# Kernel tuning notes

Measured on AMD Instinct MI355X. Metric: run time of the kernel, lower is better.

The kernel has to match this reference:

```python
import jax, jax.numpy as jnp
import numpy as np

B, N, F, H, HEADS = 2, 256, 64, 64, 4
C = HEADS * H  # n_coefficients (coefficients_mlp is Identity => must equal n_heads*hidden)
EPS = 1e-5
INF = 1e5


def _lin(key, fan_in, fan_out, bias=True):
    k1, k2 = jax.random.split(key)
    w = jax.random.normal(k1, (fan_in, fan_out), jnp.float32) * (1.0 / np.sqrt(fan_in))
    if bias:
        b = jax.random.normal(k2, (fan_out,), jnp.float32) * 0.01
        return w, b
    return w


def setup_inputs() -> dict:
    key = jax.random.key(0)
    ks = jax.random.split(key, 16)
    inp = dict(
        h=jax.random.normal(ks[0], (B, N, F), jnp.float32),
        x=jax.random.normal(ks[1], (B, N, 3), jnp.float32),
        v=jax.random.normal(ks[2], (B, N, 3), jnp.float32),
    )
    inp['edge_w1'], inp['edge_b1'] = _lin(ks[3], 2 * F + 1, H)
    inp['edge_w2'], inp['edge_b2'] = _lin(ks[4], H, H)
    inp['sem_w'], inp['sem_b'] = _lin(ks[5], H, HEADS)
    inp['post_w1'], inp['post_b1'] = _lin(ks[6], C, H)
    inp['post_w2'], inp['post_b2'] = _lin(ks[7], H, H)
    inp['node_w1'], inp['node_b1'] = _lin(ks[8], C + H + F, H)
    inp['node_w2'], inp['node_b2'] = _lin(ks[9], H, F)
    inp['vel_w1'], inp['vel_b1'] = _lin(ks[10], F, H)
    inp['vel_w2'] = _lin(ks[11], H, 1, bias=False) * 0.001  # xavier gain=0.001 analogue
    inp['vmix_w'] = _lin(ks[12], C, 1, bias=False)[:, 0]
    inp['log_gamma'] = -jnp.log(jnp.linspace(1.0, 5.0, HEADS)).astype(jnp.float32)
    return inp


def reference(h, x, v, edge_w1, edge_b1, edge_w2, edge_b2, sem_w, sem_b,
              post_w1, post_b1, post_w2, post_b2, node_w1, node_b1,
              node_w2, node_b2, vel_w1, vel_b1, vel_w2, vmix_w, log_gamma):
    silu = jax.nn.silu
    n = h.shape[-2]
    eye = jnp.eye(n, dtype=h.dtype)[:, :, None]  # [N,N,1] diagonal mask

    # pairwise geometry: entry [i,j] = x_j - x_i
    x_minus_xt = x[..., None, :, :] - x[..., :, None, :]                # [B,N,N,3]
    x_norm = jnp.sqrt((x_minus_xt ** 2).sum(-1, keepdims=True) + EPS)   # [B,N,N,1]

    # pairwise node-feature concat (h_j, h_i) + distance -> edge MLP
    h_j = jnp.broadcast_to(h[..., None, :, :], (B, n, n, F))
    h_i = jnp.broadcast_to(h[..., :, None, :], (B, n, n, F))
    h_cat = jnp.concatenate([h_j, h_i, x_norm], axis=-1)                # [B,N,N,2F+1]
    h_e_mtx = silu(silu(h_cat @ edge_w1 + edge_b1) @ edge_w2 + edge_b2)  # [B,N,N,H]

    # euclidean attention: softmin over j of gamma*dist, diagonal masked out
    dist = (x_norm + INF * eye) * jnp.exp(log_gamma)                    # [B,N,N,heads]
    euclid_att = jax.nn.softmax(-dist, axis=-2)
    # semantic attention: LeakyReLU(0.2) logits, diagonal masked, softmax over j
    sem = jax.nn.leaky_relu(h_e_mtx @ sem_w + sem_b, 0.2) - INF * eye
    sem_att = jax.nn.softmax(sem, axis=-2)
    comb_att = jax.nn.softmax(euclid_att * sem_att, axis=-2)            # [B,N,N,heads]

    # attention-weighted edge features, flattened over (H, heads)
    h_e_att = (h_e_mtx[..., :, None] * comb_att[..., None, :]).reshape(B, n, n, C)

    # spatial attention (coefficients_mlp is Identity)
    unit = x_minus_xt / (x_norm + EPS)                                  # [B,N,N,3]
    # combinations.mean(dim=-3) without materializing [B,N,N,C,3]
    comb_sum = jnp.einsum('bijc,bijd->bicd', h_e_att, unit) / n         # [B,N,C,3]
    comb_norm = (comb_sum ** 2).sum(-1)                                 # [B,N,C]
    h_comb = silu(silu(comb_norm @ post_w1 + post_b1) @ post_w2 + post_b2)

    # delta_v = mean_j (v_mixing over C of combinations)
    delta_v = jnp.einsum('bijc,c,bijd->bid', h_e_att, vmix_w, unit) / n  # [B,N,3]

    h_agg = h_e_att.sum(axis=-2)                                        # sum over j -> [B,N,C]
    out = jnp.concatenate([h, h_agg, h_comb], axis=-1)
    out = silu(silu(out @ node_w1 + node_b1) @ node_w2 + node_b2)
    h_new = h + out                                                     # residual

    # coordinate / velocity update
    v_scale = silu(h_new @ vel_w1 + vel_b1) @ vel_w2                    # [B,N,1]
    v_new = delta_v + v_scale * v
    x_new = x + v_new
    return h_new, x_new, v_new
```

## Files before the change

kernel.cpp:

```cpp
#include <hip/hip_runtime.h>
#include <hip/hip_bf16.h>
#include <math.h>

#define EPSV 1e-5f
#define INFV 1e5f

typedef short bf16x8 __attribute__((ext_vector_type(8)));
typedef float f32x4 __attribute__((ext_vector_type(4)));

__device__ __forceinline__ float rcp_f(float x) { return __builtin_amdgcn_rcpf(x); }
__device__ __forceinline__ float silu_f(float v) { return v * rcp_f(1.0f + __expf(-v)); }

__device__ __forceinline__ unsigned short f2bf(float f) {
  unsigned int u = __float_as_uint(f);
  u = (u + 0x7fffu + ((u >> 16) & 1u)) >> 16;
  return (unsigned short)u;
}
__device__ __forceinline__ float bf2f(unsigned short h) {
  return __uint_as_float(((unsigned int)h) << 16);
}
__device__ __forceinline__ unsigned int pkbf(float a, float b) {
  float2 f2; f2.x = a; f2.y = b;
  __hip_bfloat162 t = __float22bfloat162_rn(f2);
  unsigned int u;
  __builtin_memcpy(&u, &t, 4);
  return u;
}

__device__ __forceinline__ float4 br4(float4 v, int op, float4* sc) {
  const int tid = threadIdx.x;
#pragma unroll
  for (int off = 32; off >= 1; off >>= 1) {
    float ox = __shfl_xor(v.x, off);
    float oy = __shfl_xor(v.y, off);
    float oz = __shfl_xor(v.z, off);
    float ow = __shfl_xor(v.w, off);
    if (op) { v.x = fmaxf(v.x, ox); v.y = fmaxf(v.y, oy); v.z = fmaxf(v.z, oz); v.w = fmaxf(v.w, ow); }
    else    { v.x += ox; v.y += oy; v.z += oz; v.w += ow; }
  }
  if ((tid & 63) == 0) sc[tid >> 6] = v;
  __syncthreads();
  float4 r0 = sc[0], r1 = sc[1], r2 = sc[2], r3 = sc[3];
  if (op) {
    v.x = fmaxf(fmaxf(r0.x, r1.x), fmaxf(r2.x, r3.x));
    v.y = fmaxf(fmaxf(r0.y, r1.y), fmaxf(r2.y, r3.y));
    v.z = fmaxf(fmaxf(r0.z, r1.z), fmaxf(r2.z, r3.z));
    v.w = fmaxf(fmaxf(r0.w, r1.w), fmaxf(r2.w, r3.w));
  } else {
    v.x = r0.x + r1.x + r2.x + r3.x;
    v.y = r0.y + r1.y + r2.y + r3.y;
    v.z = r0.z + r1.z + r2.z + r3.z;
    v.w = r0.w + r1.w + r2.w + r3.w;
  }
  __syncthreads();
  return v;
}

__device__ __forceinline__ void gemm64(const unsigned short* TH, const unsigned short* E2T,
                                       int w, int l15, int quad, f32x4 acc[4][4]) {
#pragma unroll
  for (int tr = 0; tr < 4; ++tr)
#pragma unroll
    for (int tc = 0; tc < 4; ++tc)
      acc[tr][tc] = (f32x4){0.f, 0.f, 0.f, 0.f};
#pragma unroll
  for (int ms = 0; ms < 64; ms += 32) {
    bf16x8 af[4], bfr[4];
#pragma unroll
    for (int tr = 0; tr < 4; ++tr)
      af[tr] = *reinterpret_cast<const bf16x8*>(&TH[(64 * w + 16 * tr + l15) * 72 + ms + quad * 8]);
#pragma unroll
    for (int tc = 0; tc < 4; ++tc)
      bfr[tc] = *reinterpret_cast<const bf16x8*>(&E2T[(16 * tc + l15) * 72 + ms + quad * 8]);
#pragma unroll
    for (int tr = 0; tr < 4; ++tr)
#pragma unroll
      for (int tc = 0; tc < 4; ++tc)
        acc[tr][tc] = __builtin_amdgcn_mfma_f32_16x16x32_bf16(af[tr], bfr[tc], acc[tr][tc], 0, 0, 0);
  }
}

__global__ __launch_bounds__(256, 3) void k_all(
    const float* __restrict__ h, const float* __restrict__ x, const float* __restrict__ v,
    const float* __restrict__ ew1, const float* __restrict__ eb1,
    const float* __restrict__ ew2, const float* __restrict__ eb2,
    const float* __restrict__ semw, const float* __restrict__ semb,
    const float* __restrict__ pw1, const float* __restrict__ pb1,
    const float* __restrict__ pw2, const float* __restrict__ pb2,
    const float* __restrict__ nw1, const float* __restrict__ nb1,
    const float* __restrict__ nw2, const float* __restrict__ nb2,
    const float* __restrict__ vw1, const float* __restrict__ vb1,
    const float* __restrict__ vw2, const float* __restrict__ vmix,
    const float* __restrict__ lgam, float* __restrict__ out) {

  __shared__ __align__(16) unsigned short TH[256 * 72];
  __shared__ __align__(16) char E2u[9216];
  __shared__ __align__(16) float4 unit_l[256];
  __shared__ float addk[64];
  __shared__ float w1dk[64];
  __shared__ __align__(16) float bms[256];

  unsigned short* E2T = (unsigned short*)E2u;
  float*  sd    = (float*)E2u;
  float4* cat_l = (float4*)E2u;
  float*  cn_l  = (float*)(E2u + 4096);
  float*  hag_l = (float*)(E2u + 5120);
  float4* sc    = (float4*)(E2u + 8192);
  float*  dvs   = (float*)(E2u + 8320);
  float* tmp = (float*)TH;
  float* m1s = (float*)TH + 256;
  float* hnw = (float*)TH + 320;
  float* nin = (float*)TH + 384;

  const int bi  = blockIdx.x;
  const int i   = bi & 255;
  const int b0  = bi & ~255;
  const int tid = threadIdx.x;
  const int j   = tid;
  const int bj  = b0 | j;

  const float xi0 = x[bi * 3 + 0], xi1 = x[bi * 3 + 1], xi2 = x[bi * 3 + 2];
  const float dx = x[bj * 3 + 0] - xi0;
  const float dy = x[bj * 3 + 1] - xi1;
  const float dz = x[bj * 3 + 2] - xi2;
  const float dn = sqrtf(dx * dx + dy * dy + dz * dz + EPSV);
  const float invn = rcp_f(dn + EPSV);
  const float ux = dx * invn, uy = dy * invn, uz = dz * invn;
  unit_l[j] = make_float4(ux, uy, uz, dn);

  {
    const float4* hb4 = reinterpret_cast<const float4*>(h + (size_t)b0 * 64);
#pragma unroll
    for (int q = 0; q < 16; ++q) {
      int idx = q * 256 + tid;
      float4 f4 = hb4[idx];
      int row = idx >> 4, c4 = idx & 15;
      uint2 pk;
      pk.x = pkbf(f4.x, f4.y);
      pk.y = pkbf(f4.z, f4.w);
      *reinterpret_cast<uint2*>(&TH[row * 72 + c4 * 4]) = pk;
    }
  }
#pragma unroll
  for (int q = 0; q < 16; ++q) {
    int idx = q * 256 + tid;
    E2T[(idx & 63) * 72 + (idx >> 6)] = f2bf(ew1[idx]);
  }
  {
    int s = tid >> 6, k = tid & 63;
    const float* hrow = h + (size_t)bi * 64;
    float bp = 0.f;
#pragma unroll
    for (int f2 = 0; f2 < 16; ++f2) {
      int f = s * 16 + f2;
      bp += hrow[f] * ew1[(64 + f) * 64 + k];
    }
    bms[s * 64 + k] = bp;
  }
  __syncthreads();
  if (tid < 64) {
    addk[tid] = eb1[tid] + bms[tid] + bms[64 + tid] + bms[128 + tid] + bms[192 + tid];
    w1dk[tid] = ew1[128 * 64 + tid];
  }

  const int lid  = tid & 63;
  const int w    = tid >> 6;
  const int l15  = lid & 15;
  const int quad = lid >> 4;

  f32x4 acc[4][4];
  gemm64(TH, E2T, w, l15, quad, acc);
  __syncthreads();

#pragma unroll
  for (int tc = 0; tc < 4; ++tc) {
    float ak = addk[16 * tc + l15];
    float wd = w1dk[16 * tc + l15];
#pragma unroll
    for (int tr = 0; tr < 4; ++tr)
#pragma unroll
      for (int r = 0; r < 4; ++r) {
        int row = 64 * w + 16 * tr + quad * 4 + r;
        float val = silu_f(acc[tr][tc][r] + ak + unit_l[row].w * wd);
        TH[row * 72 + 16 * tc + l15] = f2bf(val);
      }
  }
#pragma unroll
  for (int q = 0; q < 16; ++q) {
    int idx = q * 256 + tid;
    E2T[(idx & 63) * 72 + (idx >> 6)] = f2bf(ew2[idx]);
  }
  __syncthreads();

  gemm64(TH, E2T, w, l15, quad, acc);
  __syncthreads();

#pragma unroll
  for (int tc = 0; tc < 4; ++tc) {
    float b2 = eb2[16 * tc + l15];
#pragma unroll
    for (int tr = 0; tr < 4; ++tr)
#pragma unroll
      for (int r = 0; r < 4; ++r) {
        int row = 64 * w + 16 * tr + quad * 4 + r;
        TH[row * 72 + 16 * tc + l15] = f2bf(silu_f(acc[tr][tc][r] + b2));
      }
  }
#pragma unroll
  for (int q = 0; q < 2; ++q) {
    int idx = q * 256 + tid;
    int n = idx >> 6, kk = idx & 63;
    float wv = (n < 4) ? semw[kk * 4 + n] : vmix[kk * 4 + (n - 4)];
    E2T[n * 72 + kk] = f2bf(wv);
  }
  __syncthreads();

  f32x4 acc3[4];
  {
#pragma unroll
    for (int tr = 0; tr < 4; ++tr) acc3[tr] = (f32x4){0.f, 0.f, 0.f, 0.f};
#pragma unroll
    for (int ms = 0; ms < 64; ms += 32) {
      bf16x8 b3 = *reinterpret_cast<const bf16x8*>(&E2T[l15 * 72 + ms + quad * 8]);
#pragma unroll
      for (int tr = 0; tr < 4; ++tr) {
        bf16x8 a3 = *reinterpret_cast<const bf16x8*>(&TH[(64 * w + 16 * tr + l15) * 72 + ms + quad * 8]);
        acc3[tr] = __builtin_amdgcn_mfma_f32_16x16x32_bf16(a3, b3, acc3[tr], 0, 0, 0);
      }
    }
  }
  __syncthreads();
  if (l15 < 8) {
#pragma unroll
    for (int tr = 0; tr < 4; ++tr)
#pragma unroll
      for (int r = 0; r < 4; ++r)
        sd[(64 * w + 16 * tr + quad * 4 + r) * 8 + l15] = acc3[tr][r];
  }
  __syncthreads();

  float4 s01 = *reinterpret_cast<const float4*>(sd + j * 8);
  float4 s23 = *reinterpret_cast<const float4*>(sd + j * 8 + 4);
  float4 sbv = *reinterpret_cast<const float4*>(semb);
  const float diag = (j == i) ? INFV : 0.0f;
  float4 sl;
  sl.x = s01.x + sbv.x; sl.y = s01.y + sbv.y; sl.z = s01.z + sbv.z; sl.w = s01.w + sbv.w;
  sl.x = ((sl.x > 0.f) ? sl.x : 0.2f * sl.x) - diag;
  sl.y = ((sl.y > 0.f) ? sl.y : 0.2f * sl.y) - diag;
  sl.z = ((sl.z > 0.f) ? sl.z : 0.2f * sl.z) - diag;
  sl.w = ((sl.w > 0.f) ? sl.w : 0.2f * sl.w) - diag;

  float4 lg = *reinterpret_cast<const float4*>(lgam);
  const float dni = dn + diag;
  float4 e_eu = make_float4(__expf(-dni * __expf(lg.x)), __expf(-dni * __expf(lg.y)),
                            __expf(-dni * __expf(lg.z)), __expf(-dni * __expf(lg.w)));

  float4 M = br4(sl, 1, sc);
  float4 e_sem = make_float4(__expf(sl.x - M.x), __expf(sl.y - M.y),
                             __expf(sl.z - M.z), __expf(sl.w - M.w));

  float4 a8 = e_eu, b8 = e_sem;
#pragma unroll
  for (int off = 32; off >= 1; off >>= 1) {
    a8.x += __shfl_xor(a8.x, off); a8.y += __shfl_xor(a8.y, off);
    a8.z += __shfl_xor(a8.z, off); a8.w += __shfl_xor(a8.w, off);
    b8.x += __shfl_xor(b8.x, off); b8.y += __shfl_xor(b8.y, off);
    b8.z += __shfl_xor(b8.z, off); b8.w += __shfl_xor(b8.w, off);
  }
  if ((tid & 63) == 0) { sc[tid >> 6] = a8; sc[4 + (tid >> 6)] = b8; }
  __syncthreads();
  float4 Se, Ss;
  {
    float4 r0 = sc[0], r1 = sc[1], r2 = sc[2], r3 = sc[3];
    Se = make_float4(r0.x + r1.x + r2.x + r3.x, r0.y + r1.y + r2.y + r3.y,
                     r0.z + r1.z + r2.z + r3.z, r0.w + r1.w + r2.w + r3.w);
    float4 s0 = sc[4], s1 = sc[5], s2 = sc[6], s3 = sc[7];
    Ss = make_float4(s0.x + s1.x + s2.x + s3.x, s0.y + s1.y + s2.y + s3.y,
                     s0.z + s1.z + s2.z + s3.z, s0.w + s1.w + s2.w + s3.w);
  }
  __syncthreads();

  float4 p = make_float4((e_eu.x * rcp_f(Se.x)) * (e_sem.x * rcp_f(Ss.x)),
                         (e_eu.y * rcp_f(Se.y)) * (e_sem.y * rcp_f(Ss.y)),
                         (e_eu.z * rcp_f(Se.z)) * (e_sem.z * rcp_f(Ss.z)),
                         (e_eu.w * rcp_f(Se.w)) * (e_sem.w * rcp_f(Ss.w)));
  float4 ep = make_float4(__expf(p.x), __expf(p.y), __expf(p.z), __expf(p.w));
  float4 Sp = br4(ep, 0, sc);
  float4 catt = make_float4(ep.x * rcp_f(Sp.x), ep.y * rcp_f(Sp.y),
                            ep.z * rcp_f(Sp.z), ep.w * rcp_f(Sp.w));
  cat_l[j] = catt;

  float s = catt.x * s23.x + catt.y * s23.y + catt.z * s23.z + catt.w * s23.w;
  float4 dv = br4(make_float4(s * ux, s * uy, s * uz, 0.f), 0, sc);
  if (j == 0) {
    const float inv = 1.0f / 256.0f;
    dvs[0] = dv.x * inv; dvs[1] = dv.y * inv; dvs[2] = dv.z * inv;
  }

  {
    const int kk = lid & 15;
    const int jq = lid >> 4;
    const int k  = 16 * w + kk;
    float agg[4] = {0.f, 0.f, 0.f, 0.f};
    float ax[4]  = {0.f, 0.f, 0.f, 0.f};
    float ay[4]  = {0.f, 0.f, 0.f, 0.f};
    float az[4]  = {0.f, 0.f, 0.f, 0.f};
#pragma unroll 4
    for (int jr2 = 0; jr2 < 64; ++jr2) {
      int jj = jq * 64 + ((jr2 + 4 * jq) & 63);
      float hev = bf2f(TH[jj * 72 + k]);
      float4 ca = cat_l[jj];
      float4 u  = unit_l[jj];
      float w0 = hev * ca.x, w1 = hev * ca.y, w2 = hev * ca.z, w3 = hev * ca.w;
      agg[0] += w0; agg[1] += w1; agg[2] += w2; agg[3] += w3;
      ax[0] += w0 * u.x; ay[0] += w0 * u.y; az[0] += w0 * u.z;
      ax[1] += w1 * u.x; ay[1] += w1 * u.y; az[1] += w1 * u.z;
      ax[2] += w2 * u.x; ay[2] += w2 * u.y; az[2] += w2 * u.z;
      ax[3] += w3 * u.x; ay[3] += w3 * u.y; az[3] += w3 * u.z;
    }
#pragma unroll
    for (int off = 16; off <= 32; off <<= 1) {
#pragma unroll
      for (int hd = 0; hd < 4; ++hd) {
        agg[hd] += __shfl_xor(agg[hd], off);
        ax[hd]  += __shfl_xor(ax[hd], off);
        ay[hd]  += __shfl_xor(ay[hd], off);
        az[hd]  += __shfl_xor(az[hd], off);
      }
    }
    if (jq == 0) {
      const float inv = 1.0f / 256.0f;
#pragma unroll
      for (int hd = 0; hd < 4; ++hd) {
        float cx = ax[hd] * inv, cy = ay[hd] * inv, cz = az[hd] * inv;
        cn_l[k * 4 + hd]  = cx * cx + cy * cy + cz * cz;
        hag_l[k * 4 + hd] = agg[hd];
      }
    }
  }
  __syncthreads();

  const int k = tid & 63;
  {
    float a = 0.f;
    for (int m2 = 0; m2 < 64; ++m2) {
      int m = w * 64 + m2;
      a += cn_l[m] * pw1[m * 64 + k];
    }
    tmp[tid] = a;
  }
  __syncthreads();
  if (tid < 64) m1s[tid] = silu_f(pb1[tid] + tmp[tid] + tmp[64 + tid] + tmp[128 + tid] + tmp[192 + tid]);
  __syncthreads();
  {
    float a = 0.f;
#pragma unroll
    for (int m2 = 0; m2 < 16; ++m2) {
      int m = w * 16 + m2;
      a += m1s[m] * pw2[m * 64 + k];
    }
    float hgv = hag_l[tid];
    __syncthreads();
    tmp[tid] = a;
    nin[64 + tid] = hgv;
  }
  __syncthreads();
  if (tid < 64) {
    nin[tid] = h[(size_t)bi * 64 + tid];
    nin[320 + tid] = silu_f(pb2[tid] + tmp[tid] + tmp[64 + tid] + tmp[128 + tid] + tmp[192 + tid]);
  }
  __syncthreads();
  {
    float a = 0.f;
    for (int m2 = 0; m2 < 96; ++m2) {
      int m = w * 96 + m2;
      a += nin[m] * nw1[m * 64 + k];
    }
    __syncthreads();
    tmp[tid] = a;
  }
  __syncthreads();
  if (tid < 64) m1s[tid] = silu_f(nb1[tid] + tmp[tid] + tmp[64 + tid] + tmp[128 + tid] + tmp[192 + tid]);
  __syncthreads();
  {
    float a = 0.f;
#pragma unroll
    for (int m2 = 0; m2 < 16; ++m2) {
      int m = w * 16 + m2;
      a += m1s[m] * nw2[m * 64 + k];
    }
    __syncthreads();
    tmp[tid] = a;
  }
  __syncthreads();
  if (tid < 64) {
    float hn = h[(size_t)bi * 64 + tid] +
               silu_f(nb2[tid] + tmp[tid] + tmp[64 + tid] + tmp[128 + tid] + tmp[192 + tid]);
    out[(size_t)bi * 64 + tid] = hn;
    hnw[tid] = hn;
  }
  __syncthreads();
  {
    float a = 0.f;
#pragma unroll
    for (int m2 = 0; m2 < 16; ++m2) {
      int m = w * 16 + m2;
      a += hnw[m] * vw1[m * 64 + k];
    }
    __syncthreads();
    tmp[tid] = a;
  }
  __syncthreads();
  if (tid < 64) {
    float vh = silu_f(vb1[tid] + tmp[tid] + tmp[64 + tid] + tmp[128 + tid] + tmp[192 + tid]) * vw2[tid];
#pragma unroll
    for (int off = 32; off >= 1; off >>= 1) vh += __shfl_xor(vh, off);
    if (tid == 0) {
#pragma unroll
      for (int d = 0; d < 3; ++d) {
        float vn = dvs[d] + vh * v[bi * 3 + d];
        out[32768 + bi * 3 + d] = x[bi * 3 + d] + vn;
        out[34304 + bi * 3 + d] = vn;
      }
    }
  }
}

extern "C" void kernel_launch(void* const* d_in, const int* in_sizes, int n_in,
                              void* d_out, int out_size, void* d_ws, size_t ws_size,
                              hipStream_t stream) {
  const float* h    = (const float*)d_in[0];
  const float* x    = (const float*)d_in[1];
  const float* v    = (const float*)d_in[2];
  const float* ew1  = (const float*)d_in[3];
  const float* eb1  = (const float*)d_in[4];
  const float* ew2  = (const float*)d_in[5];
  const float* eb2  = (const float*)d_in[6];
  const float* semw = (const float*)d_in[7];
  const float* semb = (const float*)d_in[8];
  const float* pw1  = (const float*)d_in[9];
  const float* pb1  = (const float*)d_in[10];
  const float* pw2  = (const float*)d_in[11];
  const float* pb2  = (const float*)d_in[12];
  const float* nw1  = (const float*)d_in[13];
  const float* nb1  = (const float*)d_in[14];
  const float* nw2  = (const float*)d_in[15];
  const float* nb2  = (const float*)d_in[16];
  const float* vw1  = (const float*)d_in[17];
  const float* vb1  = (const float*)d_in[18];
  const float* vw2  = (const float*)d_in[19];
  const float* vmix = (const float*)d_in[20];
  const float* lgam = (const float*)d_in[21];
  float* out = (float*)d_out;

  k_all<<<512, 256, 0, stream>>>(h, x, v, ew1, eb1, ew2, eb2, semw, semb,
                                 pw1, pb1, pw2, pb2, nw1, nb1, nw2, nb2,
                                 vw1, vb1, vw2, vmix, lgam, out);
}
```

Baseline: 121.9 us.

## Double block to 512 threads and split per-node work across eight waves

Launches 512-thread blocks and re-partitions every stage across 8 wavefronts. The edge-MLP MFMA tiles shrink to 32 rows per wave, and the first GEMM is transposed so its output is written as packed bf16 quads. The aggregation loop, the post/node/velocity MLP mat-vecs and the partial-sum reductions are all split eight ways. The aim is more waves per CU to hide latency, since the grid has only 512 blocks. In exchange, the upper half of the block redundantly recomputes the per-j softmax work, and the eight-way LDS reductions add extra barrier steps.

```diff
diff --git a/kernel.cpp b/kernel.cpp
--- a/kernel.cpp
+++ b/kernel.cpp
@@ -27,7 +27,7 @@
   return u;
 }
 
-__device__ __forceinline__ float4 br4(float4 v, int op, float4* sc) {
+__device__ __forceinline__ float4 br8(float4 v, int op, float4* sc) {
   const int tid = threadIdx.x;
 #pragma unroll
   for (int off = 32; off >= 1; off >>= 1) {
@@ -38,7 +38,7 @@
     if (op) { v.x = fmaxf(v.x, ox); v.y = fmaxf(v.y, oy); v.z = fmaxf(v.z, oz); v.w = fmaxf(v.w, ow); }
     else    { v.x += ox; v.y += oy; v.z += oz; v.w += ow; }
   }
-  if ((tid & 63) == 0) sc[tid >> 6] = v;
+  if ((tid & 63) == 0 && (tid >> 6) < 4) sc[tid >> 6] = v;
   __syncthreads();
   float4 r0 = sc[0], r1 = sc[1], r2 = sc[2], r3 = sc[3];
   if (op) {
@@ -56,31 +56,7 @@
   return v;
 }
 
-__device__ __forceinline__ void gemm64(const unsigned short* TH, const unsigned short* E2T,
-                                       int w, int l15, int quad, f32x4 acc[4][4]) {
-#pragma unroll
-  for (int tr = 0; tr < 4; ++tr)
-#pragma unroll
-    for (int tc = 0; tc < 4; ++tc)
-      acc[tr][tc] = (f32x4){0.f, 0.f, 0.f, 0.f};
-#pragma unroll
-  for (int ms = 0; ms < 64; ms += 32) {
-    bf16x8 af[4], bfr[4];
-#pragma unroll
-    for (int tr = 0; tr < 4; ++tr)
-      af[tr] = *reinterpret_cast<const bf16x8*>(&TH[(64 * w + 16 * tr + l15) * 72 + ms + quad * 8]);
-#pragma unroll
-    for (int tc = 0; tc < 4; ++tc)
-      bfr[tc] = *reinterpret_cast<const bf16x8*>(&E2T[(16 * tc + l15) * 72 + ms + quad * 8]);
-#pragma unroll
-    for (int tr = 0; tr < 4; ++tr)
-#pragma unroll
-      for (int tc = 0; tc < 4; ++tc)
-        acc[tr][tc] = __builtin_amdgcn_mfma_f32_16x16x32_bf16(af[tr], bfr[tc], acc[tr][tc], 0, 0, 0);
-  }
-}
-
-__global__ __launch_bounds__(256, 3) void k_all(
+__global__ __launch_bounds__(512, 4) void k_all(
     const float* __restrict__ h, const float* __restrict__ x, const float* __restrict__ v,
     const float* __restrict__ ew1, const float* __restrict__ eb1,
     const float* __restrict__ ew2, const float* __restrict__ eb2,
@@ -96,9 +72,9 @@
   __shared__ __align__(16) unsigned short TH[256 * 72];
   __shared__ __align__(16) char E2u[9216];
   __shared__ __align__(16) float4 unit_l[256];
-  __shared__ float addk[64];
-  __shared__ float w1dk[64];
-  __shared__ __align__(16) float bms[256];
+  __shared__ __align__(16) float bms[512];
+  __shared__ __align__(16) float addk[64];
+  __shared__ __align__(16) float w1dk[64];
 
   unsigned short* E2T = (unsigned short*)E2u;
   float*  sd    = (float*)E2u;
@@ -106,18 +82,21 @@
   float*  cn_l  = (float*)(E2u + 4096);
   float*  hag_l = (float*)(E2u + 5120);
   float4* sc    = (float4*)(E2u + 8192);
-  float*  dvs   = (float*)(E2u + 8320);
   float* tmp = (float*)TH;
-  float* m1s = (float*)TH + 256;
-  float* hnw = (float*)TH + 320;
-  float* nin = (float*)TH + 384;
+  float* m1s = (float*)TH + 512;
+  float* hnw = (float*)TH + 576;
+  float* nin = (float*)TH + 640;
 
   const int bi  = blockIdx.x;
   const int i   = bi & 255;
   const int b0  = bi & ~255;
   const int tid = threadIdx.x;
-  const int j   = tid;
-  const int bj  = b0 | j;
+  const int w    = tid >> 6;
+  const int lid  = tid & 63;
+  const int l15  = lid & 15;
+  const int quad = lid >> 4;
+  const int j8   = tid & 255;
+  const int bj   = b0 | j8;
 
   const float xi0 = x[bi * 3 + 0], xi1 = x[bi * 3 + 1], xi2 = x[bi * 3 + 2];
   const float dx = x[bj * 3 + 0] - xi0;
@@ -126,13 +105,13 @@
   const float dn = sqrtf(dx * dx + dy * dy + dz * dz + EPSV);
   const float invn = rcp_f(dn + EPSV);
   const float ux = dx * invn, uy = dy * invn, uz = dz * invn;
-  unit_l[j] = make_float4(ux, uy, uz, dn);
+  unit_l[j8] = make_float4(ux, uy, uz, dn);
 
   {
     const float4* hb4 = reinterpret_cast<const float4*>(h + (size_t)b0 * 64);
 #pragma unroll
-    for (int q = 0; q < 16; ++q) {
-      int idx = q * 256 + tid;
+    for (int q = 0; q < 8; ++q) {
+      int idx = q * 512 + tid;
       float4 f4 = hb4[idx];
       int row = idx >> 4, c4 = idx & 15;
       uint2 pk;
@@ -142,172 +121,209 @@
     }
   }
 #pragma unroll
-  for (int q = 0; q < 16; ++q) {
-    int idx = q * 256 + tid;
+  for (int q = 0; q < 8; ++q) {
+    int idx = q * 512 + tid;
     E2T[(idx & 63) * 72 + (idx >> 6)] = f2bf(ew1[idx]);
   }
   {
-    int s = tid >> 6, k = tid & 63;
+    int s = tid >> 6, k0 = tid & 63;
     const float* hrow = h + (size_t)bi * 64;
     float bp = 0.f;
 #pragma unroll
-    for (int f2 = 0; f2 < 16; ++f2) {
-      int f = s * 16 + f2;
-      bp += hrow[f] * ew1[(64 + f) * 64 + k];
-    }
-    bms[s * 64 + k] = bp;
-  }
-  __syncthreads();
-  if (tid < 64) {
-    addk[tid] = eb1[tid] + bms[tid] + bms[64 + tid] + bms[128 + tid] + bms[192 + tid];
+    for (int f2 = 0; f2 < 8; ++f2) {
+      int f = s * 8 + f2;
+      bp += hrow[f] * ew1[(64 + f) * 64 + k0];
+    }
+    bms[s * 64 + k0] = bp;
+  }
+  __syncthreads();
+  if (tid < 64) {
+    float a = eb1[tid];
+#pragma unroll
+    for (int s2 = 0; s2 < 8; ++s2) a += bms[s2 * 64 + tid];
+    addk[tid] = a;
     w1dk[tid] = ew1[128 * 64 + tid];
   }
 
-  const int lid  = tid & 63;
-  const int w    = tid >> 6;
-  const int l15  = lid & 15;
-  const int quad = lid >> 4;
-
-  f32x4 acc[4][4];
-  gemm64(TH, E2T, w, l15, quad, acc);
-  __syncthreads();
-
-#pragma unroll
-  for (int tc = 0; tc < 4; ++tc) {
-    float ak = addk[16 * tc + l15];
-    float wd = w1dk[16 * tc + l15];
-#pragma unroll
-    for (int tr = 0; tr < 4; ++tr)
-#pragma unroll
-      for (int r = 0; r < 4; ++r) {
-        int row = 64 * w + 16 * tr + quad * 4 + r;
-        float val = silu_f(acc[tr][tc][r] + ak + unit_l[row].w * wd);
-        TH[row * 72 + 16 * tc + l15] = f2bf(val);
-      }
-  }
-#pragma unroll
-  for (int q = 0; q < 16; ++q) {
-    int idx = q * 256 + tid;
+  f32x4 acc1[4][2];
+#pragma unroll
+  for (int tm = 0; tm < 4; ++tm)
+#pragma unroll
+    for (int tn = 0; tn < 2; ++tn) acc1[tm][tn] = (f32x4){0.f, 0.f, 0.f, 0.f};
+#pragma unroll
+  for (int ms = 0; ms < 64; ms += 32) {
+    bf16x8 am[4], bn[2];
+#pragma unroll
+    for (int tm = 0; tm < 4; ++tm)
+      am[tm] = *reinterpret_cast<const bf16x8*>(&E2T[(16 * tm + l15) * 72 + ms + quad * 8]);
+#pragma unroll
+    for (int tn = 0; tn < 2; ++tn)
+      bn[tn] = *reinterpret_cast<const bf16x8*>(&TH[(32 * w + 16 * tn + l15) * 72 + ms + quad * 8]);
+#pragma unroll
+    for (int tm = 0; tm < 4; ++tm)
+#pragma unroll
+      for (int tn = 0; tn < 2; ++tn)
+        acc1[tm][tn] = __builtin_amdgcn_mfma_f32_16x16x32_bf16(am[tm], bn[tn], acc1[tm][tn], 0, 0, 0);
+  }
+  __syncthreads();
+
+#pragma unroll
+  for (int tn = 0; tn < 2; ++tn) {
+    int j = 32 * w + 16 * tn + l15;
+    float dnj = unit_l[j].w;
+#pragma unroll
+    for (int tm = 0; tm < 4; ++tm) {
+      float4 ad = *reinterpret_cast<const float4*>(&addk[16 * tm + 4 * quad]);
+      float4 wd = *reinterpret_cast<const float4*>(&w1dk[16 * tm + 4 * quad]);
+      float v0 = silu_f(acc1[tm][tn][0] + ad.x + dnj * wd.x);
+      float v1 = silu_f(acc1[tm][tn][1] + ad.y + dnj * wd.y);
+      float v2 = silu_f(acc1[tm][tn][2] + ad.z + dnj * wd.z);
+      float v3 = silu_f(acc1[tm][tn][3] + ad.w + dnj * wd.w);
+      uint2 pk;
+      pk.x = pkbf(v0, v1);
+      pk.y = pkbf(v2, v3);
+      *reinterpret_cast<uint2*>(&TH[j * 72 + 16 * tm + 4 * quad]) = pk;
+    }
+  }
+#pragma unroll
+  for (int q = 0; q < 8; ++q) {
+    int idx = q * 512 + tid;
     E2T[(idx & 63) * 72 + (idx >> 6)] = f2bf(ew2[idx]);
   }
   __syncthreads();
 
-  gemm64(TH, E2T, w, l15, quad, acc);
+  f32x4 acc2[2][4];
+#pragma unroll
+  for (int tr = 0; tr < 2; ++tr)
+#pragma unroll
+    for (int tc = 0; tc < 4; ++tc) acc2[tr][tc] = (f32x4){0.f, 0.f, 0.f, 0.f};
+#pragma unroll
+  for (int ms = 0; ms < 64; ms += 32) {
+    bf16x8 af[2], bfr[4];
+#pragma unroll
+    for (int tr = 0; tr < 2; ++tr)
+      af[tr] = *reinterpret_cast<const bf16x8*>(&TH[(32 * w + 16 * tr + l15) * 72 + ms + quad * 8]);
+#pragma unroll
+    for (int tc = 0; tc < 4; ++tc)
+      bfr[tc] = *reinterpret_cast<const bf16x8*>(&E2T[(16 * tc + l15) * 72 + ms + quad * 8]);
+#pragma unroll
+    for (int tr = 0; tr < 2; ++tr)
+#pragma unroll
+      for (int tc = 0; tc < 4; ++tc)
+        acc2[tr][tc] = __builtin_amdgcn_mfma_f32_16x16x32_bf16(af[tr], bfr[tc], acc2[tr][tc], 0, 0, 0);
+  }
   __syncthreads();
 
 #pragma unroll
   for (int tc = 0; tc < 4; ++tc) {
     float b2 = eb2[16 * tc + l15];
 #pragma unroll
-    for (int tr = 0; tr < 4; ++tr)
+    for (int tr = 0; tr < 2; ++tr)
 #pragma unroll
       for (int r = 0; r < 4; ++r) {
-        int row = 64 * w + 16 * tr + quad * 4 + r;
-        TH[row * 72 + 16 * tc + l15] = f2bf(silu_f(acc[tr][tc][r] + b2));
+        int row = 32 * w + 16 * tr + quad * 4 + r;
+        TH[row * 72 + 16 * tc + l15] = f2bf(silu_f(acc2[tr][tc][r] + b2));
       }
   }
-#pragma unroll
-  for (int q = 0; q < 2; ++q) {
-    int idx = q * 256 + tid;
-    int n = idx >> 6, kk = idx & 63;
+  {
+    int n = tid >> 6, kk = tid & 63;
     float wv = (n < 4) ? semw[kk * 4 + n] : vmix[kk * 4 + (n - 4)];
     E2T[n * 72 + kk] = f2bf(wv);
   }
   __syncthreads();
 
-  f32x4 acc3[4];
-  {
-#pragma unroll
-    for (int tr = 0; tr < 4; ++tr) acc3[tr] = (f32x4){0.f, 0.f, 0.f, 0.f};
-#pragma unroll
-    for (int ms = 0; ms < 64; ms += 32) {
-      bf16x8 b3 = *reinterpret_cast<const bf16x8*>(&E2T[l15 * 72 + ms + quad * 8]);
-#pragma unroll
-      for (int tr = 0; tr < 4; ++tr) {
-        bf16x8 a3 = *reinterpret_cast<const bf16x8*>(&TH[(64 * w + 16 * tr + l15) * 72 + ms + quad * 8]);
-        acc3[tr] = __builtin_amdgcn_mfma_f32_16x16x32_bf16(a3, b3, acc3[tr], 0, 0, 0);
-      }
+  f32x4 acc3[2];
+  acc3[0] = (f32x4){0.f, 0.f, 0.f, 0.f};
+  acc3[1] = (f32x4){0.f, 0.f, 0.f, 0.f};
+#pragma unroll
+  for (int ms = 0; ms < 64; ms += 32) {
+    bf16x8 b3 = *reinterpret_cast<const bf16x8*>(&E2T[l15 * 72 + ms + quad * 8]);
+#pragma unroll
+    for (int tr = 0; tr < 2; ++tr) {
+      bf16x8 a3 = *reinterpret_cast<const bf16x8*>(&TH[(32 * w + 16 * tr + l15) * 72 + ms + quad * 8]);
+      acc3[tr] = __builtin_amdgcn_mfma_f32_16x16x32_bf16(a3, b3, acc3[tr], 0, 0, 0);
     }
   }
   __syncthreads();
   if (l15 < 8) {
 #pragma unroll
-    for (int tr = 0; tr < 4; ++tr)
+    for (int tr = 0; tr < 2; ++tr)
 #pragma unroll
       for (int r = 0; r < 4; ++r)
-        sd[(64 * w + 16 * tr + quad * 4 + r) * 8 + l15] = acc3[tr][r];
-  }
-  __syncthreads();
-
-  float4 s01 = *reinterpret_cast<const float4*>(sd + j * 8);
-  float4 s23 = *reinterpret_cast<const float4*>(sd + j * 8 + 4);
-  float4 sbv = *reinterpret_cast<const float4*>(semb);
-  const float diag = (j == i) ? INFV : 0.0f;
-  float4 sl;
-  sl.x = s01.x + sbv.x; sl.y = s01.y + sbv.y; sl.z = s01.z + sbv.z; sl.w = s01.w + sbv.w;
-  sl.x = ((sl.x > 0.f) ? sl.x : 0.2f * sl.x) - diag;
-  sl.y = ((sl.y > 0.f) ? sl.y : 0.2f * sl.y) - diag;
-  sl.z = ((sl.z > 0.f) ? sl.z : 0.2f * sl.z) - diag;
-  sl.w = ((sl.w > 0.f) ? sl.w : 0.2f * sl.w) - diag;
-
-  float4 lg = *reinterpret_cast<const float4*>(lgam);
-  const float dni = dn + diag;
-  float4 e_eu = make_float4(__expf(-dni * __expf(lg.x)), __expf(-dni * __expf(lg.y)),
-                            __expf(-dni * __expf(lg.z)), __expf(-dni * __expf(lg.w)));
-
-  float4 M = br4(sl, 1, sc);
-  float4 e_sem = make_float4(__expf(sl.x - M.x), __expf(sl.y - M.y),
-                             __expf(sl.z - M.z), __expf(sl.w - M.w));
-
-  float4 a8 = e_eu, b8 = e_sem;
-#pragma unroll
-  for (int off = 32; off >= 1; off >>= 1) {
-    a8.x += __shfl_xor(a8.x, off); a8.y += __shfl_xor(a8.y, off);
-    a8.z += __shfl_xor(a8.z, off); a8.w += __shfl_xor(a8.w, off);
-    b8.x += __shfl_xor(b8.x, off); b8.y += __shfl_xor(b8.y, off);
-    b8.z += __shfl_xor(b8.z, off); b8.w += __shfl_xor(b8.w, off);
-  }
-  if ((tid & 63) == 0) { sc[tid >> 6] = a8; sc[4 + (tid >> 6)] = b8; }
-  __syncthreads();
-  float4 Se, Ss;
-  {
-    float4 r0 = sc[0], r1 = sc[1], r2 = sc[2], r3 = sc[3];
-    Se = make_float4(r0.x + r1.x + r2.x + r3.x, r0.y + r1.y + r2.y + r3.y,
-                     r0.z + r1.z + r2.z + r3.z, r0.w + r1.w + r2.w + r3.w);
-    float4 s0 = sc[4], s1 = sc[5], s2 = sc[6], s3 = sc[7];
-    Ss = make_float4(s0.x + s1.x + s2.x + s3.x, s0.y + s1.y + s2.y + s3.y,
-                     s0.z + s1.z + s2.z + s3.z, s0.w + s1.w + s2.w + s3.w);
-  }
-  __syncthreads();
-
-  float4 p = make_float4((e_eu.x * rcp_f(Se.x)) * (e_sem.x * rcp_f(Ss.x)),
-                         (e_eu.y * rcp_f(Se.y)) * (e_sem.y * rcp_f(Ss.y)),
-                         (e_eu.z * rcp_f(Se.z)) * (e_sem.z * rcp_f(Ss.z)),
-                         (e_eu.w * rcp_f(Se.w)) * (e_sem.w * rcp_f(Ss.w)));
-  float4 ep = make_float4(__expf(p.x), __expf(p.y), __expf(p.z), __expf(p.w));
-  float4 Sp = br4(ep, 0, sc);
-  float4 catt = make_float4(ep.x * rcp_f(Sp.x), ep.y * rcp_f(Sp.y),
-                            ep.z * rcp_f(Sp.z), ep.w * rcp_f(Sp.w));
-  cat_l[j] = catt;
-
-  float s = catt.x * s23.x + catt.y * s23.y + catt.z * s23.z + catt.w * s23.w;
-  float4 dv = br4(make_float4(s * ux, s * uy, s * uz, 0.f), 0, sc);
-  if (j == 0) {
+        sd[(32 * w + 16 * tr + quad * 4 + r) * 8 + l15] = acc3[tr][r];
+  }
+  __syncthreads();
+
+  float dv0 = 0.f, dv1 = 0.f, dv2 = 0.f;
+  {
+    float4 s01 = *reinterpret_cast<const float4*>(sd + j8 * 8);
+    float4 s23 = *reinterpret_cast<const float4*>(sd + j8 * 8 + 4);
+    float4 sbv = *reinterpret_cast<const float4*>(semb);
+    const float diag = (j8 == i) ? INFV : 0.0f;
+    float4 sl;
+    sl.x = s01.x + sbv.x; sl.y = s01.y + sbv.y; sl.z = s01.z + sbv.z; sl.w = s01.w + sbv.w;
+    sl.x = ((sl.x > 0.f) ? sl.x : 0.2f * sl.x) - diag;
+    sl.y = ((sl.y > 0.f) ? sl.y : 0.2f * sl.y) - diag;
+    sl.z = ((sl.z > 0.f) ? sl.z : 0.2f * sl.z) - diag;
+    sl.w = ((sl.w > 0.f) ? sl.w : 0.2f * sl.w) - diag;
+
+    float4 lg = *reinterpret_cast<const float4*>(lgam);
+    const float dni = dn + diag;
+    float4 e_eu = make_float4(__expf(-dni * __expf(lg.x)), __expf(-dni * __expf(lg.y)),
+                              __expf(-dni * __expf(lg.z)), __expf(-dni * __expf(lg.w)));
+
+    float4 M = br8(sl, 1, sc);
+    float4 e_sem = make_float4(__expf(sl.x - M.x), __expf(sl.y - M.y),
+                               __expf(sl.z - M.z), __expf(sl.w - M.w));
+
+    float4 a8 = e_eu, b8 = e_sem;
+#pragma unroll
+    for (int off = 32; off >= 1; off >>= 1) {
+      a8.x += __shfl_xor(a8.x, off); a8.y += __shfl_xor(a8.y, off);
+      a8.z += __shfl_xor(a8.z, off); a8.w += __shfl_xor(a8.w, off);
+      b8.x += __shfl_xor(b8.x, off); b8.y += __shfl_xor(b8.y, off);
+      b8.z += __shfl_xor(b8.z, off); b8.w += __shfl_xor(b8.w, off);
+    }
+    if ((tid & 63) == 0 && w < 4) { sc[w] = a8; sc[4 + w] = b8; }
+    __syncthreads();
+    float4 Se, Ss;
+    {
+      float4 r0 = sc[0], r1 = sc[1], r2 = sc[2], r3 = sc[3];
+      Se = make_float4(r0.x + r1.x + r2.x + r3.x, r0.y + r1.y + r2.y + r3.y,
+                       r0.z + r1.z + r2.z + r3.z, r0.w + r1.w + r2.w + r3.w);
+      float4 s0 = sc[4], s1 = sc[5], s2 = sc[6], s3 = sc[7];
+      Ss = make_float4(s0.x + s1.x + s2.x + s3.x, s0.y + s1.y + s2.y + s3.y,
+                       s0.z + s1.z + s2.z + s3.z, s0.w + s1.w + s2.w + s3.w);
+    }
+    __syncthreads();
+
+    float4 p = make_float4((e_eu.x * rcp_f(Se.x)) * (e_sem.x * rcp_f(Ss.x)),
+                           (e_eu.y * rcp_f(Se.y)) * (e_sem.y * rcp_f(Ss.y)),
+                           (e_eu.z * rcp_f(Se.z)) * (e_sem.z * rcp_f(Ss.z)),
+                           (e_eu.w * rcp_f(Se.w)) * (e_sem.w * rcp_f(Ss.w)));
+    float4 ep = make_float4(__expf(p.x), __expf(p.y), __expf(p.z), __expf(p.w));
+    float4 Sp = br8(ep, 0, sc);
+    float4 catt = make_float4(ep.x * rcp_f(Sp.x), ep.y * rcp_f(Sp.y),
+                              ep.z * rcp_f(Sp.z), ep.w * rcp_f(Sp.w));
+    cat_l[j8] = catt;
+
+    float s = catt.x * s23.x + catt.y * s23.y + catt.z * s23.z + catt.w * s23.w;
+    float4 dv = br8(make_float4(s * ux, s * uy, s * uz, 0.f), 0, sc);
     const float inv = 1.0f / 256.0f;
-    dvs[0] = dv.x * inv; dvs[1] = dv.y * inv; dvs[2] = dv.z * inv;
-  }
-
-  {
-    const int kk = lid & 15;
-    const int jq = lid >> 4;
-    const int k  = 16 * w + kk;
+    dv0 = dv.x * inv; dv1 = dv.y * inv; dv2 = dv.z * inv;
+  }
+
+  {
+    const int g  = lid >> 3;
+    const int jq = lid & 7;
+    const int k  = 8 * w + g;
     float agg[4] = {0.f, 0.f, 0.f, 0.f};
     float ax[4]  = {0.f, 0.f, 0.f, 0.f};
     float ay[4]  = {0.f, 0.f, 0.f, 0.f};
     float az[4]  = {0.f, 0.f, 0.f, 0.f};
 #pragma unroll 4
-    for (int jr2 = 0; jr2 < 64; ++jr2) {
-      int jj = jq * 64 + ((jr2 + 4 * jq) & 63);
+    for (int it = 0; it < 32; ++it) {
+      int jj = 32 * jq + ((it + jq) & 31);
       float hev = bf2f(TH[jj * 72 + k]);
       float4 ca = cat_l[jj];
       float4 u  = unit_l[jj];
@@ -319,7 +335,7 @@
       ax[3] += w3 * u.x; ay[3] += w3 * u.y; az[3] += w3 * u.z;
     }
 #pragma unroll
-    for (int off = 16; off <= 32; off <<= 1) {
+    for (int off = 1; off <= 4; off <<= 1) {
 #pragma unroll
       for (int hd = 0; hd < 4; ++hd) {
         agg[hd] += __shfl_xor(agg[hd], off);
@@ -340,62 +356,77 @@
   }
   __syncthreads();
 
-  const int k = tid & 63;
+  const int k0 = tid & 63;
   {
     float a = 0.f;
-    for (int m2 = 0; m2 < 64; ++m2) {
-      int m = w * 64 + m2;
-      a += cn_l[m] * pw1[m * 64 + k];
+    for (int m2 = 0; m2 < 32; ++m2) {
+      int m = w * 32 + m2;
+      a += cn_l[m] * pw1[m * 64 + k0];
     }
     tmp[tid] = a;
   }
   __syncthreads();
-  if (tid < 64) m1s[tid] = silu_f(pb1[tid] + tmp[tid] + tmp[64 + tid] + tmp[128 + tid] + tmp[192 + tid]);
+  if (tid < 64) {
+    float a = pb1[tid];
+#pragma unroll
+    for (int s2 = 0; s2 < 8; ++s2) a += tmp[tid + 64 * s2];
+    m1s[tid] = silu_f(a);
+  }
   __syncthreads();
   {
     float a = 0.f;
 #pragma unroll
-    for (int m2 = 0; m2 < 16; ++m2) {
-      int m = w * 16 + m2;
-      a += m1s[m] * pw2[m * 64 + k];
-    }
-    float hgv = hag_l[tid];
+    for (int m2 = 0; m2 < 8; ++m2) {
+      int m = w * 8 + m2;
+      a += m1s[m] * pw2[m * 64 + k0];
+    }
+    float hgv = hag_l[j8];
     __syncthreads();
     tmp[tid] = a;
-    nin[64 + tid] = hgv;
-  }
-  __syncthreads();
-  if (tid < 64) {
+    nin[64 + j8] = hgv;
+  }
+  __syncthreads();
+  if (tid < 64) {
+    float a = pb2[tid];
+#pragma unroll
+    for (int s2 = 0; s2 < 8; ++s2) a += tmp[tid + 64 * s2];
     nin[tid] = h[(size_t)bi * 64 + tid];
-    nin[320 + tid] = silu_f(pb2[tid] + tmp[tid] + tmp[64 + tid] + tmp[128 + tid] + tmp[192 + tid]);
+    nin[320 + tid] = silu_f(a);
   }
   __syncthreads();
   {
     float a = 0.f;
-    for (int m2 = 0; m2 < 96; ++m2) {
-      int m = w * 96 + m2;
-      a += nin[m] * nw1[m * 64 + k];
+    for (int m2 = 0; m2 < 48; ++m2) {
+      int m = w * 48 + m2;
+      a += nin[m] * nw1[m * 64 + k0];
     }
     __syncthreads();
     tmp[tid] = a;
   }
   __syncthreads();
-  if (tid < 64) m1s[tid] = silu_f(nb1[tid] + tmp[tid] + tmp[64 + tid] + tmp[128 + tid] + tmp[192 + tid]);
+  if (tid < 64) {
+    float a = nb1[tid];
+#pragma unroll
+    for (int s2 = 0; s2 < 8; ++s2) a += tmp[tid + 64 * s2];
+    m1s[tid] = silu_f(a);
+  }
   __syncthreads();
   {
     float a = 0.f;
 #pragma unroll
-    for (int m2 = 0; m2 < 16; ++m2) {
-      int m = w * 16 + m2;
-      a += m1s[m] * nw2[m * 64 + k];
+    for (int m2 = 0; m2 < 8; ++m2) {
+      int m = w * 8 + m2;
+      a += m1s[m] * nw2[m * 64 + k0];
     }
     __syncthreads();
     tmp[tid] = a;
   }
   __syncthreads();
   if (tid < 64) {
-    float hn = h[(size_t)bi * 64 + tid] +
-               silu_f(nb2[tid] + tmp[tid] + tmp[64 + tid] + tmp[128 + tid] + tmp[192 + tid]);
+    float a = nb2[tid];
+#pragma unroll
+    for (int s2 = 0; s2 < 8; ++s2) a += tmp[tid + 64 * s2];
+    float hn = h[(size_t)bi * 64 + tid] + silu_f(a);
     out[(size_t)bi * 64 + tid] = hn;
     hnw[tid] = hn;
   }
@@ -403,22 +434,26 @@
   {
     float a = 0.f;
 #pragma unroll
-    for (int m2 = 0; m2 < 16; ++m2) {
-      int m = w * 16 + m2;
-      a += hnw[m] * vw1[m * 64 + k];
+    for (int m2 = 0; m2 < 8; ++m2) {
+      int m = w * 8 + m2;
+      a += hnw[m] * vw1[m * 64 + k0];
     }
     __syncthreads();
     tmp[tid] = a;
   }
   __syncthreads();
   if (tid < 64) {
-    float vh = silu_f(vb1[tid] + tmp[tid] + tmp[64 + tid] + tmp[128 + tid] + tmp[192 + tid]) * vw2[tid];
+    float a = vb1[tid];
+#pragma unroll
+    for (int s2 = 0; s2 < 8; ++s2) a += tmp[tid + 64 * s2];
+    float vh = silu_f(a) * vw2[tid];
 #pragma unroll
     for (int off = 32; off >= 1; off >>= 1) vh += __shfl_xor(vh, off);
     if (tid == 0) {
+      float dvv[3] = {dv0, dv1, dv2};
 #pragma unroll
       for (int d = 0; d < 3; ++d) {
-        float vn = dvs[d] + vh * v[bi * 3 + d];
+        float vn = dvv[d] + vh * v[bi * 3 + d];
         out[32768 + bi * 3 + d] = x[bi * 3 + d] + vn;
         out[34304 + bi * 3 + d] = vn;
       }
@@ -453,7 +488,7 @@
   const float* lgam = (const float*)d_in[21];
   float* out = (float*)d_out;
 
-  k_all<<<512, 256, 0, stream>>>(h, x, v, ew1, eb1, ew2, eb2, semw, semb,
+  k_all<<<512, 512, 0, stream>>>(h, x, v, ew1, eb1, ew2, eb2, semw, semb,
                                  pw1, pb1, pw2, pb2, nw1, nb1, nw2, nb2,
                                  vw1, vb1, vw2, vmix, lgam, out);
 }
```

After: 124.0 us. No clear change (+1.7%).
